# Optimization experiments

Hardware: AMD Instinct MI355X
Metric: run time of the kernel (lower is better)

## Reference

```python
import jax, jax.numpy as jnp
import numpy as np

N_X = 20000      # bessel x-grid
N_ELL = 48       # sparse tabulated multipoles
N_K = 1024       # k quadrature points
N_TAU = 600      # conformal-time samples
K_PIVOT = 0.05


def fast_interp(x, xmin, xmax, ytab):
    """Uniform-grid linear interpolation (tools.fast_interp). ytab: [Nx]."""
    n = ytab.shape[0]
    pos = jnp.clip((x - xmin) / (xmax - xmin) * (n - 1), 0.0, n - 1.0)
    i0 = jnp.clip(jnp.floor(pos).astype(jnp.int32), 0, n - 2)
    w = pos - i0
    return ytab[i0] * (1.0 - w) + ytab[i0 + 1] * w


def setup_inputs() -> dict:
    key = jax.random.key(0)
    ks = jax.random.split(key, 8)
    k = jnp.logspace(-4.0, 0.0, N_K, dtype=jnp.float32)           # Mpc^-1
    tau = jnp.linspace(50.0, 14000.0, N_TAU, dtype=jnp.float32)    # Mpc
    tau0 = jnp.asarray(14100.0, dtype=jnp.float32)
    bessel_x_tab = jnp.linspace(0.0, 15000.0, N_X, dtype=jnp.float32)
    mk = lambda kk, sh, s: (s * jax.random.normal(kk, sh, dtype=jnp.float32))
    return {
        "k": k,
        "tau": tau,
        "tau0": tau0,
        "S0": mk(ks[0], (N_K, N_TAU), 1e-2),
        "S1": mk(ks[1], (N_K, N_TAU), 1e-2),
        "S2": mk(ks[2], (N_K, N_TAU), 1e-2),
        "SE": mk(ks[3], (N_K, N_TAU), 1e-2),
        "bessel_x_tab": bessel_x_tab,
        "phi0_tab": mk(ks[4], (N_X, N_ELL), 1e-1),
        "phi1_tab": mk(ks[5], (N_X, N_ELL), 1e-1),
        "phi2_tab": mk(ks[6], (N_X, N_ELL), 1e-1),
        "eps_tab": mk(ks[7], (N_X, N_ELL), 1e-1),
        "A_s": jnp.asarray(2.1e-9, dtype=jnp.float32),
        "n_s": jnp.asarray(0.965, dtype=jnp.float32),
    }


def reference(k, tau, tau0, S0, S1, S2, SE, bessel_x_tab,
              phi0_tab, phi1_tab, phi2_tab, eps_tab, A_s, n_s):
    xmin = bessel_x_tab[0]
    xmax = bessel_x_tab[-1]
    # radial argument x = k * (tau0 - tau): [K, T]
    x = k[:, None] * (tau0 - tau)[None, :]

    def one_ell(p0, p1, p2, pe):
        # lookup phi0/phi1/phi2/epsilon at every (k, tau), fuse with sources
        srcT = (S0 * fast_interp(x, xmin, xmax, p0)
                + S1 * fast_interp(x, xmin, xmax, p1)
                + S2 * fast_interp(x, xmin, xmax, p2))
        Tl = jnp.trapezoid(srcT, tau, axis=-1)                       # [K]
        El = jnp.trapezoid(SE * fast_interp(x, xmin, xmax, pe), tau, axis=-1)
        return Tl, El

    # vmap over the tabulated-ell axis (columns of the Bessel tables)
    Tl, El = jax.vmap(one_ell, in_axes=(1, 1, 1, 1))(
        phi0_tab, phi1_tab, phi2_tab, eps_tab)                       # [L, K]

    # primordial curvature spectrum P_R(k) = A_s (k/k_p)^(n_s-1) * 2 pi^2 / k^3
    P_R = A_s * (k / K_PIVOT) ** (n_s - 1.0) * (2.0 * jnp.pi ** 2 / k ** 3)
    w = k * k * P_R                                                   # [K]
    c = 2.0 / jnp.pi
    ClTT = c * jnp.trapezoid(w * Tl * Tl, k, axis=-1)                 # [L]
    ClEE = c * jnp.trapezoid(w * El * El, k, axis=-1)
    ClTE = c * jnp.trapezoid(w * Tl * El, k, axis=-1)
    return jnp.stack([ClTT, ClEE, ClTE], axis=0)                      # [3, L]
```

## Files before the change

### kernel.cpp

```cpp
#include <hip/hip_runtime.h>
#include <math.h>

#define N_X   20000
#define N_ELL 48
#define N_K   1024
#define N_TAU 600
#define SPLIT 4
#define CHUNK (N_TAU / SPLIT)

__device__ __forceinline__ unsigned int pack_half2(float lo, float hi) {
    _Float16 l = (_Float16)lo, h = (_Float16)hi;
    unsigned short lu = __builtin_bit_cast(unsigned short, l);
    unsigned short hu = __builtin_bit_cast(unsigned short, h);
    return (unsigned int)lu | ((unsigned int)hu << 16);
}
__device__ __forceinline__ float fdot2(unsigned int a, unsigned int b, float c) {
    float d;
    asm("v_dot2_f32_f16 %0, %1, %2, %3" : "=v"(d) : "v"(a), "v"(b), "v"(c));
    return d;
}

__global__ __launch_bounds__(256) void repack_kernel(
    const float* __restrict__ p0, const float* __restrict__ p1,
    const float* __restrict__ p2, const float* __restrict__ pe,
    uint4* __restrict__ P)
{
    const int total = N_X * N_ELL;
    for (int idx = blockIdx.x * blockDim.x + threadIdx.x; idx < total;
         idx += gridDim.x * blockDim.x) {
        int x = idx / N_ELL;
        int e = idx - x * N_ELL;
        int xn = (x < N_X - 1) ? x + 1 : x;
        int a = x * N_ELL + e, b = xn * N_ELL + e;
        uint4 v;
        v.x = pack_half2(p0[a], p0[b]);
        v.y = pack_half2(p1[a], p1[b]);
        v.z = pack_half2(p2[a], p2[b]);
        v.w = pack_half2(pe[a], pe[b]);
        P[idx] = v;
    }
}

__global__ __launch_bounds__(256) void tl_el_packed(
    const float* __restrict__ k, const float* __restrict__ tau,
    const float* __restrict__ tau0p,
    const float* __restrict__ S0, const float* __restrict__ S1,
    const float* __restrict__ S2, const float* __restrict__ SE,
    const float* __restrict__ bx, const uint4* __restrict__ P,
    float* __restrict__ Tlp, float* __restrict__ Elp)
{
    const int bid  = blockIdx.x;
    const int part = bid & (SPLIT - 1);
    const int kidx = (N_K - 1) - (bid >> 2);
    const int t0   = part * CHUNK;
    const int tid  = threadIdx.x;
    const int wave = tid >> 6;
    const int lane = tid & 63;
    const int ell  = (lane < N_ELL) ? lane : (N_ELL - 1);

    __shared__ unsigned int off_s[CHUNK];
    __shared__ uint4        W2_s[CHUNK];
    __shared__ float        redT[4][N_ELL];
    __shared__ float        redE[4][N_ELL];

    const float kk    = k[kidx];
    const float tau0  = tau0p[0];
    const float xmin  = bx[0];
    const float xmax  = bx[N_X - 1];
    const float scale = (float)(N_X - 1) / (xmax - xmin);

    if (tid < CHUNK) {
        int t = t0 + tid;
        float tt = tau[t];
        float tp = (t > 0)         ? tau[t - 1] : tt;
        float tn = (t < N_TAU - 1) ? tau[t + 1] : tt;
        float wt = 0.5f * (tn - tp);
        float x   = kk * (tau0 - tt);
        float pos = (x - xmin) * scale;
        pos = fminf(fmaxf(pos, 0.0f), (float)(N_X - 1));
        int i0 = (int)pos;
        if (i0 > N_X - 2) i0 = N_X - 2;
        float w  = pos - (float)i0;
        float om = 1.0f - w;
        size_t sb = (size_t)kidx * N_TAU + t;
        float s0 = wt * S0[sb], s1 = wt * S1[sb];
        float s2 = wt * S2[sb], se = wt * SE[sb];
        uint4 w2;
        w2.x = pack_half2(s0 * om, s0 * w);
        w2.y = pack_half2(s1 * om, s1 * w);
        w2.z = pack_half2(s2 * om, s2 * w);
        w2.w = pack_half2(se * om, se * w);
        W2_s[tid]  = w2;
        off_s[tid] = (unsigned int)i0 * (N_ELL * 16u);
    }
    __syncthreads();

    const char* Pb = (const char*)P;
    const unsigned int elloff = (unsigned int)ell * 16u;
    float aT0 = 0.0f, aT1 = 0.0f, aT2 = 0.0f, aE = 0.0f;

    #pragma unroll 4
    for (int i = wave; i < CHUNK; i += 4) {
        unsigned int voff = off_s[i] + elloff;
        uint4 pr = *(const uint4*)(Pb + voff);
        uint4 w2 = W2_s[i];
        aT0 = fdot2(pr.x, w2.x, aT0);
        aT1 = fdot2(pr.y, w2.y, aT1);
        aT2 = fdot2(pr.z, w2.z, aT2);
        aE  = fdot2(pr.w, w2.w, aE);
    }
    float accT = (aT0 + aT1) + aT2;

    if (lane < N_ELL) { redT[wave][lane] = accT; redE[wave][lane] = aE; }
    __syncthreads();
    if (tid < N_ELL) {
        float sT = (redT[0][tid] + redT[1][tid]) + (redT[2][tid] + redT[3][tid]);
        float sE = (redE[0][tid] + redE[1][tid]) + (redE[2][tid] + redE[3][tid]);
        Tlp[((size_t)part * N_ELL + tid) * N_K + kidx] = sT;
        Elp[((size_t)part * N_ELL + tid) * N_K + kidx] = sE;
    }
}

__global__ __launch_bounds__(256) void tl_el_kernel(
    const float* __restrict__ k, const float* __restrict__ tau,
    const float* __restrict__ tau0p,
    const float* __restrict__ S0, const float* __restrict__ S1,
    const float* __restrict__ S2, const float* __restrict__ SE,
    const float* __restrict__ bx,
    const float* __restrict__ p0, const float* __restrict__ p1,
    const float* __restrict__ p2, const float* __restrict__ pe,
    float* __restrict__ Tl, float* __restrict__ El)
{
    const int kidx = blockIdx.x;
    const int tid  = threadIdx.x;
    const int wave = tid >> 6;
    const int lane = tid & 63;
    const int ell  = (lane < N_ELL) ? lane : (N_ELL - 1);

    const float kk    = k[kidx];
    const float tau0  = tau0p[0];
    const float xmin  = bx[0];
    const float xmax  = bx[N_X - 1];
    const float scale = (float)(N_X - 1) / (xmax - xmin);

    const float* Srow0 = S0 + (size_t)kidx * N_TAU;
    const float* Srow1 = S1 + (size_t)kidx * N_TAU;
    const float* Srow2 = S2 + (size_t)kidx * N_TAU;
    const float* SrowE = SE + (size_t)kidx * N_TAU;

    float accT = 0.0f, accE = 0.0f;

    for (int t = wave; t < N_TAU; t += 4) {
        float tt    = tau[t];
        float tprev = (t > 0)         ? tau[t - 1] : tt;
        float tnext = (t < N_TAU - 1) ? tau[t + 1] : tt;
        float wt    = 0.5f * (tnext - tprev);

        float x   = kk * (tau0 - tt);
        float pos = (x - xmin) * scale;
        pos = fminf(fmaxf(pos, 0.0f), (float)(N_X - 1));
        int i0 = (int)floorf(pos);
        if (i0 > N_X - 2) i0 = N_X - 2;
        float w = pos - (float)i0;

        int base = i0 * N_ELL + ell;
        float y00 = p0[base], y01 = p0[base + N_ELL];
        float y10 = p1[base], y11 = p1[base + N_ELL];
        float y20 = p2[base], y21 = p2[base + N_ELL];
        float ye0 = pe[base], ye1 = pe[base + N_ELL];

        float a0 = fmaf(w, y01 - y00, y00);
        float a1 = fmaf(w, y11 - y10, y10);
        float a2 = fmaf(w, y21 - y20, y20);
        float ae = fmaf(w, ye1 - ye0, ye0);

        float s0 = Srow0[t], s1 = Srow1[t], s2 = Srow2[t], se = SrowE[t];

        float srcT = s0 * a0 + s1 * a1 + s2 * a2;
        accT = fmaf(wt, srcT, accT);
        accE = fmaf(wt, se * ae, accE);
    }

    __shared__ float redT[4][N_ELL];
    __shared__ float redE[4][N_ELL];
    if (lane < N_ELL) { redT[wave][lane] = accT; redE[wave][lane] = accE; }
    __syncthreads();
    if (tid < N_ELL) {
        float sT = (redT[0][tid] + redT[1][tid]) + (redT[2][tid] + redT[3][tid]);
        float sE = (redE[0][tid] + redE[1][tid]) + (redE[2][tid] + redE[3][tid]);
        Tl[tid * N_K + kidx] = sT;
        El[tid * N_K + kidx] = sE;
    }
}

__global__ __launch_bounds__(256) void cl_kernel(
    const float* __restrict__ k,
    const float* __restrict__ Asp, const float* __restrict__ nsp,
    const float* __restrict__ Tlp, const float* __restrict__ Elp,
    int nparts, float* __restrict__ out)
{
    const int ell = blockIdx.x;
    const int tid = threadIdx.x;
    const float A_s = Asp[0];
    const float n_s = nsp[0];
    const float two_pi2 = 2.0f * (float)M_PI * (float)M_PI;

    float aTT = 0.0f, aEE = 0.0f, aTE = 0.0f;
    for (int i = tid; i < N_K; i += 256) {
        float kv    = k[i];
        float kprev = (i > 0)       ? k[i - 1] : kv;
        float knext = (i < N_K - 1) ? k[i + 1] : kv;
        float dkw   = 0.5f * (knext - kprev);
        float Pw = A_s * powf(kv / 0.05f, n_s - 1.0f) * two_pi2 / kv;
        float ww = dkw * Pw;
        float tl = 0.0f, el = 0.0f;
        for (int p = 0; p < nparts; ++p) {
            tl += Tlp[((size_t)p * N_ELL + ell) * N_K + i];
            el += Elp[((size_t)p * N_ELL + ell) * N_K + i];
        }
        aTT = fmaf(ww * tl, tl, aTT);
        aEE = fmaf(ww * el, el, aEE);
        aTE = fmaf(ww * tl, el, aTE);
    }

    for (int off = 32; off > 0; off >>= 1) {
        aTT += __shfl_down(aTT, off, 64);
        aEE += __shfl_down(aEE, off, 64);
        aTE += __shfl_down(aTE, off, 64);
    }
    __shared__ float red[3][4];
    const int wave = tid >> 6, lane = tid & 63;
    if (lane == 0) { red[0][wave] = aTT; red[1][wave] = aEE; red[2][wave] = aTE; }
    __syncthreads();
    if (tid == 0) {
        const float c = 2.0f / (float)M_PI;
        out[0 * N_ELL + ell] = c * ((red[0][0] + red[0][1]) + (red[0][2] + red[0][3]));
        out[1 * N_ELL + ell] = c * ((red[1][0] + red[1][1]) + (red[1][2] + red[1][3]));
        out[2 * N_ELL + ell] = c * ((red[2][0] + red[2][1]) + (red[2][2] + red[2][3]));
    }
}

extern "C" void kernel_launch(void* const* d_in, const int* in_sizes, int n_in,
                              void* d_out, int out_size, void* d_ws, size_t ws_size,
                              hipStream_t stream) {
    const float* k    = (const float*)d_in[0];
    const float* tau  = (const float*)d_in[1];
    const float* tau0 = (const float*)d_in[2];
    const float* S0   = (const float*)d_in[3];
    const float* S1   = (const float*)d_in[4];
    const float* S2   = (const float*)d_in[5];
    const float* SE   = (const float*)d_in[6];
    const float* bx   = (const float*)d_in[7];
    const float* p0   = (const float*)d_in[8];
    const float* p1   = (const float*)d_in[9];
    const float* p2   = (const float*)d_in[10];
    const float* pe   = (const float*)d_in[11];
    const float* A_s  = (const float*)d_in[12];
    const float* n_s  = (const float*)d_in[13];
    float* out = (float*)d_out;

    const size_t P_bytes    = (size_t)N_X * N_ELL * sizeof(uint4);
    const size_t part_bytes = (size_t)SPLIT * N_ELL * N_K * sizeof(float);

    if (ws_size >= P_bytes + 2 * part_bytes) {
        uint4* P   = (uint4*)d_ws;
        float* Tlp = (float*)((char*)d_ws + P_bytes);
        float* Elp = (float*)((char*)d_ws + P_bytes + part_bytes);

        repack_kernel<<<(N_X * N_ELL + 255) / 256, 256, 0, stream>>>(p0, p1, p2, pe, P);
        tl_el_packed<<<N_K * SPLIT, 256, 0, stream>>>(k, tau, tau0, S0, S1, S2, SE, bx,
                                                      P, Tlp, Elp);
        cl_kernel<<<N_ELL, 256, 0, stream>>>(k, A_s, n_s, Tlp, Elp, SPLIT, out);
    } else {
        float* Tl = (float*)d_ws;
        float* El = Tl + (size_t)N_ELL * N_K;
        tl_el_kernel<<<N_K, 256, 0, stream>>>(k, tau, tau0, S0, S1, S2, SE, bx,
                                              p0, p1, p2, pe, Tl, El);
        cl_kernel<<<N_ELL, 256, 0, stream>>>(k, A_s, n_s, Tl, El, 1, out);
    }
}
```

Before: 135.2 us.

## Pack Bessel tables as 8-byte rows and split Cl reduction across k-chunks

The repacked table now stores the four Bessel tables interleaved per x as half precision (8 bytes) instead of duplicating the neighbour row (16 bytes), which halves the table footprint and the repack traffic. The main kernel does two 8-byte loads (row i0 and row i0+1) and uses zero-padded dot2 weights to pull out the per-table contributions. The Cl kernel is also spread over a 2D grid of ell by k-chunk and combines partial sums with atomicAdd into an output that the repack kernel zeroes. This costs an extra load instruction per tau point and more dot2 ops, and the atomic accumulation makes the summation order nondeterministic.

```diff
diff --git a/kernel.cpp b/kernel.cpp
--- a/kernel.cpp
+++ b/kernel.cpp
@@ -7,6 +7,8 @@
 #define N_TAU 600
 #define SPLIT 4
 #define CHUNK (N_TAU / SPLIT)
+#define ROWB  (N_ELL * 8)
+#define KCH   4
 
 __device__ __forceinline__ unsigned int pack_half2(float lo, float hi) {
     _Float16 l = (_Float16)lo, h = (_Float16)hi;
@@ -20,23 +22,18 @@
     return d;
 }
 
-__global__ __launch_bounds__(256) void repack_kernel(
+__global__ __launch_bounds__(256) void repack_kernel2(
     const float* __restrict__ p0, const float* __restrict__ p1,
     const float* __restrict__ p2, const float* __restrict__ pe,
-    uint4* __restrict__ P)
-{
+    uint2* __restrict__ P, float* __restrict__ out)
+{
+    if (blockIdx.x == 0 && threadIdx.x < 3 * N_ELL) out[threadIdx.x] = 0.0f;
     const int total = N_X * N_ELL;
     for (int idx = blockIdx.x * blockDim.x + threadIdx.x; idx < total;
          idx += gridDim.x * blockDim.x) {
-        int x = idx / N_ELL;
-        int e = idx - x * N_ELL;
-        int xn = (x < N_X - 1) ? x + 1 : x;
-        int a = x * N_ELL + e, b = xn * N_ELL + e;
-        uint4 v;
-        v.x = pack_half2(p0[a], p0[b]);
-        v.y = pack_half2(p1[a], p1[b]);
-        v.z = pack_half2(p2[a], p2[b]);
-        v.w = pack_half2(pe[a], pe[b]);
+        uint2 v;
+        v.x = pack_half2(p0[idx], p1[idx]);
+        v.y = pack_half2(p2[idx], pe[idx]);
         P[idx] = v;
     }
 }
@@ -46,7 +43,7 @@
     const float* __restrict__ tau0p,
     const float* __restrict__ S0, const float* __restrict__ S1,
     const float* __restrict__ S2, const float* __restrict__ SE,
-    const float* __restrict__ bx, const uint4* __restrict__ P,
+    const float* __restrict__ bx, const uint2* __restrict__ P,
     float* __restrict__ Tlp, float* __restrict__ Elp)
 {
     const int bid  = blockIdx.x;
@@ -59,7 +56,8 @@
     const int ell  = (lane < N_ELL) ? lane : (N_ELL - 1);
 
     __shared__ unsigned int off_s[CHUNK];
-    __shared__ uint4        W2_s[CHUNK];
+    __shared__ uint4        WT_s[CHUNK];
+    __shared__ uint2        WE_s[CHUNK];
     __shared__ float        redT[4][N_ELL];
     __shared__ float        redE[4][N_ELL];
 
@@ -80,38 +78,48 @@
         pos = fminf(fmaxf(pos, 0.0f), (float)(N_X - 1));
         int i0 = (int)pos;
         if (i0 > N_X - 2) i0 = N_X - 2;
-        float w  = pos - (float)i0;
-        float om = 1.0f - w;
+        float w   = pos - (float)i0;
+        float clo = wt * (1.0f - w);
+        float chi = wt * w;
         size_t sb = (size_t)kidx * N_TAU + t;
-        float s0 = wt * S0[sb], s1 = wt * S1[sb];
-        float s2 = wt * S2[sb], se = wt * SE[sb];
-        uint4 w2;
-        w2.x = pack_half2(s0 * om, s0 * w);
-        w2.y = pack_half2(s1 * om, s1 * w);
-        w2.z = pack_half2(s2 * om, s2 * w);
-        w2.w = pack_half2(se * om, se * w);
-        W2_s[tid]  = w2;
-        off_s[tid] = (unsigned int)i0 * (N_ELL * 16u);
+        float s0 = S0[sb], s1 = S1[sb], s2 = S2[sb], se = SE[sb];
+        uint4 wt4;
+        wt4.x = pack_half2(clo * s0, clo * s1);
+        wt4.y = pack_half2(chi * s0, chi * s1);
+        wt4.z = pack_half2(clo * s2, 0.0f);
+        wt4.w = pack_half2(chi * s2, 0.0f);
+        uint2 we2;
+        we2.x = pack_half2(0.0f, clo * se);
+        we2.y = pack_half2(0.0f, chi * se);
+        WT_s[tid]  = wt4;
+        WE_s[tid]  = we2;
+        off_s[tid] = (unsigned int)i0 * (unsigned int)ROWB;
     }
     __syncthreads();
 
     const char* Pb = (const char*)P;
-    const unsigned int elloff = (unsigned int)ell * 16u;
-    float aT0 = 0.0f, aT1 = 0.0f, aT2 = 0.0f, aE = 0.0f;
+    const unsigned int elloff = (unsigned int)ell * 8u;
+    float aT0 = 0.0f, aT1 = 0.0f, aT2 = 0.0f, aT3 = 0.0f;
+    float aE0 = 0.0f, aE1 = 0.0f;
 
     #pragma unroll 4
     for (int i = wave; i < CHUNK; i += 4) {
         unsigned int voff = off_s[i] + elloff;
-        uint4 pr = *(const uint4*)(Pb + voff);
-        uint4 w2 = W2_s[i];
-        aT0 = fdot2(pr.x, w2.x, aT0);
-        aT1 = fdot2(pr.y, w2.y, aT1);
-        aT2 = fdot2(pr.z, w2.z, aT2);
-        aE  = fdot2(pr.w, w2.w, aE);
-    }
-    float accT = (aT0 + aT1) + aT2;
-
-    if (lane < N_ELL) { redT[wave][lane] = accT; redE[wave][lane] = aE; }
+        uint2 lo = *(const uint2*)(Pb + voff);
+        uint2 hi = *(const uint2*)(Pb + voff + ROWB);
+        uint4 wt4 = WT_s[i];
+        uint2 we2 = WE_s[i];
+        aT0 = fdot2(lo.x, wt4.x, aT0);
+        aT1 = fdot2(hi.x, wt4.y, aT1);
+        aT2 = fdot2(lo.y, wt4.z, aT2);
+        aT3 = fdot2(hi.y, wt4.w, aT3);
+        aE0 = fdot2(lo.y, we2.x, aE0);
+        aE1 = fdot2(hi.y, we2.y, aE1);
+    }
+    float accT = (aT0 + aT1) + (aT2 + aT3);
+    float accE = aE0 + aE1;
+
+    if (lane < N_ELL) { redT[wave][lane] = accT; redE[wave][lane] = accE; }
     __syncthreads();
     if (tid < N_ELL) {
         float sT = (redT[0][tid] + redT[1][tid]) + (redT[2][tid] + redT[3][tid]);
@@ -193,35 +201,35 @@
     }
 }
 
-__global__ __launch_bounds__(256) void cl_kernel(
+__global__ __launch_bounds__(256) void cl_kernel2(
     const float* __restrict__ k,
     const float* __restrict__ Asp, const float* __restrict__ nsp,
     const float* __restrict__ Tlp, const float* __restrict__ Elp,
     int nparts, float* __restrict__ out)
 {
-    const int ell = blockIdx.x;
-    const int tid = threadIdx.x;
+    const int ell   = blockIdx.x;
+    const int chunk = blockIdx.y;
+    const int tid   = threadIdx.x;
+    const int i     = chunk * 256 + tid;
     const float A_s = Asp[0];
     const float n_s = nsp[0];
     const float two_pi2 = 2.0f * (float)M_PI * (float)M_PI;
 
-    float aTT = 0.0f, aEE = 0.0f, aTE = 0.0f;
-    for (int i = tid; i < N_K; i += 256) {
-        float kv    = k[i];
-        float kprev = (i > 0)       ? k[i - 1] : kv;
-        float knext = (i < N_K - 1) ? k[i + 1] : kv;
-        float dkw   = 0.5f * (knext - kprev);
-        float Pw = A_s * powf(kv / 0.05f, n_s - 1.0f) * two_pi2 / kv;
-        float ww = dkw * Pw;
-        float tl = 0.0f, el = 0.0f;
-        for (int p = 0; p < nparts; ++p) {
-            tl += Tlp[((size_t)p * N_ELL + ell) * N_K + i];
-            el += Elp[((size_t)p * N_ELL + ell) * N_K + i];
-        }
-        aTT = fmaf(ww * tl, tl, aTT);
-        aEE = fmaf(ww * el, el, aEE);
-        aTE = fmaf(ww * tl, el, aTE);
-    }
+    float kv    = k[i];
+    float kprev = (i > 0)       ? k[i - 1] : kv;
+    float knext = (i < N_K - 1) ? k[i + 1] : kv;
+    float dkw   = 0.5f * (knext - kprev);
+    float Pw    = A_s * powf(kv / 0.05f, n_s - 1.0f) * two_pi2 / kv;
+    float ww    = dkw * Pw;
+
+    float tl = 0.0f, el = 0.0f;
+    for (int p = 0; p < nparts; ++p) {
+        tl += Tlp[((size_t)p * N_ELL + ell) * N_K + i];
+        el += Elp[((size_t)p * N_ELL + ell) * N_K + i];
+    }
+    float aTT = ww * tl * tl;
+    float aEE = ww * el * el;
+    float aTE = ww * tl * el;
 
     for (int off = 32; off > 0; off >>= 1) {
         aTT += __shfl_down(aTT, off, 64);
@@ -234,9 +242,12 @@
     __syncthreads();
     if (tid == 0) {
         const float c = 2.0f / (float)M_PI;
-        out[0 * N_ELL + ell] = c * ((red[0][0] + red[0][1]) + (red[0][2] + red[0][3]));
-        out[1 * N_ELL + ell] = c * ((red[1][0] + red[1][1]) + (red[1][2] + red[1][3]));
-        out[2 * N_ELL + ell] = c * ((red[2][0] + red[2][1]) + (red[2][2] + red[2][3]));
+        atomicAdd(&out[0 * N_ELL + ell],
+                  c * ((red[0][0] + red[0][1]) + (red[0][2] + red[0][3])));
+        atomicAdd(&out[1 * N_ELL + ell],
+                  c * ((red[1][0] + red[1][1]) + (red[1][2] + red[1][3])));
+        atomicAdd(&out[2 * N_ELL + ell],
+                  c * ((red[2][0] + red[2][1]) + (red[2][2] + red[2][3])));
     }
 }
 
@@ -259,23 +270,26 @@
     const float* n_s  = (const float*)d_in[13];
     float* out = (float*)d_out;
 
-    const size_t P_bytes    = (size_t)N_X * N_ELL * sizeof(uint4);
+    const size_t P_bytes    = (size_t)N_X * N_ELL * sizeof(uint2);
     const size_t part_bytes = (size_t)SPLIT * N_ELL * N_K * sizeof(float);
 
     if (ws_size >= P_bytes + 2 * part_bytes) {
-        uint4* P   = (uint4*)d_ws;
+        uint2* P   = (uint2*)d_ws;
         float* Tlp = (float*)((char*)d_ws + P_bytes);
         float* Elp = (float*)((char*)d_ws + P_bytes + part_bytes);
 
-        repack_kernel<<<(N_X * N_ELL + 255) / 256, 256, 0, stream>>>(p0, p1, p2, pe, P);
+        repack_kernel2<<<(N_X * N_ELL + 255) / 256, 256, 0, stream>>>(
+            p0, p1, p2, pe, P, out);
         tl_el_packed<<<N_K * SPLIT, 256, 0, stream>>>(k, tau, tau0, S0, S1, S2, SE, bx,
                                                       P, Tlp, Elp);
-        cl_kernel<<<N_ELL, 256, 0, stream>>>(k, A_s, n_s, Tlp, Elp, SPLIT, out);
+        cl_kernel2<<<dim3(N_ELL, KCH), 256, 0, stream>>>(k, A_s, n_s, Tlp, Elp,
+                                                         SPLIT, out);
     } else {
         float* Tl = (float*)d_ws;
         float* El = Tl + (size_t)N_ELL * N_K;
+        hipMemsetAsync(out, 0, 3 * N_ELL * sizeof(float), stream);
         tl_el_kernel<<<N_K, 256, 0, stream>>>(k, tau, tau0, S0, S1, S2, SE, bx,
                                               p0, p1, p2, pe, Tl, El);
-        cl_kernel<<<N_ELL, 256, 0, stream>>>(k, A_s, n_s, Tl, El, 1, out);
-    }
-}
+        cl_kernel2<<<dim3(N_ELL, KCH), 256, 0, stream>>>(k, A_s, n_s, Tl, El, 1, out);
+    }
+}
```

Measured after the change: 141.7 us. 1.05x slower.

## Double-buffer gather loads in tl_el and split Cl reduction across k-chunks with atomics

Applied to the files above, without the earlier changes.

The main tau loop now issues batches of eight 16-byte table gathers into two register buffers, with scheduling barriers so that loads for one batch are in flight while the previous batch is consumed. The shared arrays are padded to 160 entries with zero weights so the fixed five-batch schedule needs no bounds checks. The Cl kernel is also spread over a 2D grid of ell by k-chunk and combines its partial sums with atomicAdd into an output zeroed in the repack kernel, which raises block count for the final reduction. The cost is higher register pressure, a little wasted work on the padded entries, and a summation order that is no longer deterministic.

```diff
diff --git a/kernel.cpp b/kernel.cpp
--- a/kernel.cpp
+++ b/kernel.cpp
@@ -7,6 +7,9 @@
 #define N_TAU 600
 #define SPLIT 4
 #define CHUNK (N_TAU / SPLIT)
+#define ROWB  (N_ELL * 16)
+#define KCH   4
+#define PADN  160
 
 __device__ __forceinline__ unsigned int pack_half2(float lo, float hi) {
     _Float16 l = (_Float16)lo, h = (_Float16)hi;
@@ -23,8 +26,9 @@
 __global__ __launch_bounds__(256) void repack_kernel(
     const float* __restrict__ p0, const float* __restrict__ p1,
     const float* __restrict__ p2, const float* __restrict__ pe,
-    uint4* __restrict__ P)
+    uint4* __restrict__ P, float* __restrict__ out)
 {
+    if (blockIdx.x == 0 && threadIdx.x < 3 * N_ELL) out[threadIdx.x] = 0.0f;
     const int total = N_X * N_ELL;
     for (int idx = blockIdx.x * blockDim.x + threadIdx.x; idx < total;
          idx += gridDim.x * blockDim.x) {
@@ -58,8 +62,8 @@
     const int lane = tid & 63;
     const int ell  = (lane < N_ELL) ? lane : (N_ELL - 1);
 
-    __shared__ unsigned int off_s[CHUNK];
-    __shared__ uint4        W2_s[CHUNK];
+    __shared__ unsigned int off_s[PADN];
+    __shared__ uint4        WT_s[PADN];
     __shared__ float        redT[4][N_ELL];
     __shared__ float        redE[4][N_ELL];
 
@@ -90,8 +94,12 @@
         w2.y = pack_half2(s1 * om, s1 * w);
         w2.z = pack_half2(s2 * om, s2 * w);
         w2.w = pack_half2(se * om, se * w);
-        W2_s[tid]  = w2;
-        off_s[tid] = (unsigned int)i0 * (N_ELL * 16u);
+        WT_s[tid]  = w2;
+        off_s[tid] = (unsigned int)i0 * (unsigned int)ROWB;
+    } else if (tid < PADN) {
+        uint4 z4; z4.x = z4.y = z4.z = z4.w = 0u;
+        WT_s[tid]  = z4;
+        off_s[tid] = 0u;
     }
     __syncthreads();
 
@@ -99,16 +107,40 @@
     const unsigned int elloff = (unsigned int)ell * 16u;
     float aT0 = 0.0f, aT1 = 0.0f, aT2 = 0.0f, aE = 0.0f;
 
-    #pragma unroll 4
-    for (int i = wave; i < CHUNK; i += 4) {
-        unsigned int voff = off_s[i] + elloff;
-        uint4 pr = *(const uint4*)(Pb + voff);
-        uint4 w2 = W2_s[i];
-        aT0 = fdot2(pr.x, w2.x, aT0);
-        aT1 = fdot2(pr.y, w2.y, aT1);
-        aT2 = fdot2(pr.z, w2.z, aT2);
-        aE  = fdot2(pr.w, w2.w, aE);
-    }
+    uint4 A[8], B[8];
+
+#define ISSUE(BUF, G)                                                      \
+    _Pragma("unroll")                                                      \
+    for (int m = 0; m < 8; ++m) {                                          \
+        unsigned int voff = off_s[wave + 4 * m + 32 * (G)] + elloff;       \
+        BUF[m] = *(const uint4*)(Pb + voff);                               \
+    }
+
+#define CONSUME(BUF, G)                                                    \
+    _Pragma("unroll")                                                      \
+    for (int m = 0; m < 8; ++m) {                                          \
+        int idx = wave + 4 * m + 32 * (G);                                 \
+        uint4 w2 = WT_s[idx];                                              \
+        aT0 = fdot2(BUF[m].x, w2.x, aT0);                                  \
+        aT1 = fdot2(BUF[m].y, w2.y, aT1);                                  \
+        aT2 = fdot2(BUF[m].z, w2.z, aT2);                                  \
+        aE  = fdot2(BUF[m].w, w2.w, aE);                                   \
+    }
+
+#define SB __builtin_amdgcn_sched_barrier(0)
+
+    ISSUE(A, 0); SB;
+    ISSUE(B, 1); SB;
+    CONSUME(A, 0); ISSUE(A, 2); SB;
+    CONSUME(B, 1); ISSUE(B, 3); SB;
+    CONSUME(A, 2); ISSUE(A, 4); SB;
+    CONSUME(B, 3); SB;
+    CONSUME(A, 4);
+
+#undef ISSUE
+#undef CONSUME
+#undef SB
+
     float accT = (aT0 + aT1) + aT2;
 
     if (lane < N_ELL) { redT[wave][lane] = accT; redE[wave][lane] = aE; }
@@ -193,35 +225,35 @@
     }
 }
 
-__global__ __launch_bounds__(256) void cl_kernel(
+__global__ __launch_bounds__(256) void cl_kernel2(
     const float* __restrict__ k,
     const float* __restrict__ Asp, const float* __restrict__ nsp,
     const float* __restrict__ Tlp, const float* __restrict__ Elp,
     int nparts, float* __restrict__ out)
 {
-    const int ell = blockIdx.x;
-    const int tid = threadIdx.x;
+    const int ell   = blockIdx.x;
+    const int chunk = blockIdx.y;
+    const int tid   = threadIdx.x;
+    const int i     = chunk * 256 + tid;
     const float A_s = Asp[0];
     const float n_s = nsp[0];
     const float two_pi2 = 2.0f * (float)M_PI * (float)M_PI;
 
-    float aTT = 0.0f, aEE = 0.0f, aTE = 0.0f;
-    for (int i = tid; i < N_K; i += 256) {
-        float kv    = k[i];
-        float kprev = (i > 0)       ? k[i - 1] : kv;
-        float knext = (i < N_K - 1) ? k[i + 1] : kv;
-        float dkw   = 0.5f * (knext - kprev);
-        float Pw = A_s * powf(kv / 0.05f, n_s - 1.0f) * two_pi2 / kv;
-        float ww = dkw * Pw;
-        float tl = 0.0f, el = 0.0f;
-        for (int p = 0; p < nparts; ++p) {
-            tl += Tlp[((size_t)p * N_ELL + ell) * N_K + i];
-            el += Elp[((size_t)p * N_ELL + ell) * N_K + i];
-        }
-        aTT = fmaf(ww * tl, tl, aTT);
-        aEE = fmaf(ww * el, el, aEE);
-        aTE = fmaf(ww * tl, el, aTE);
-    }
+    float kv    = k[i];
+    float kprev = (i > 0)       ? k[i - 1] : kv;
+    float knext = (i < N_K - 1) ? k[i + 1] : kv;
+    float dkw   = 0.5f * (knext - kprev);
+    float Pw    = A_s * powf(kv / 0.05f, n_s - 1.0f) * two_pi2 / kv;
+    float ww    = dkw * Pw;
+
+    float tl = 0.0f, el = 0.0f;
+    for (int p = 0; p < nparts; ++p) {
+        tl += Tlp[((size_t)p * N_ELL + ell) * N_K + i];
+        el += Elp[((size_t)p * N_ELL + ell) * N_K + i];
+    }
+    float aTT = ww * tl * tl;
+    float aEE = ww * el * el;
+    float aTE = ww * tl * el;
 
     for (int off = 32; off > 0; off >>= 1) {
         aTT += __shfl_down(aTT, off, 64);
@@ -234,9 +266,12 @@
     __syncthreads();
     if (tid == 0) {
         const float c = 2.0f / (float)M_PI;
-        out[0 * N_ELL + ell] = c * ((red[0][0] + red[0][1]) + (red[0][2] + red[0][3]));
-        out[1 * N_ELL + ell] = c * ((red[1][0] + red[1][1]) + (red[1][2] + red[1][3]));
-        out[2 * N_ELL + ell] = c * ((red[2][0] + red[2][1]) + (red[2][2] + red[2][3]));
+        atomicAdd(&out[0 * N_ELL + ell],
+                  c * ((red[0][0] + red[0][1]) + (red[0][2] + red[0][3])));
+        atomicAdd(&out[1 * N_ELL + ell],
+                  c * ((red[1][0] + red[1][1]) + (red[1][2] + red[1][3])));
+        atomicAdd(&out[2 * N_ELL + ell],
+                  c * ((red[2][0] + red[2][1]) + (red[2][2] + red[2][3])));
     }
 }
 
@@ -267,15 +302,18 @@
         float* Tlp = (float*)((char*)d_ws + P_bytes);
         float* Elp = (float*)((char*)d_ws + P_bytes + part_bytes);
 
-        repack_kernel<<<(N_X * N_ELL + 255) / 256, 256, 0, stream>>>(p0, p1, p2, pe, P);
+        repack_kernel<<<(N_X * N_ELL + 255) / 256, 256, 0, stream>>>(
+            p0, p1, p2, pe, P, out);
         tl_el_packed<<<N_K * SPLIT, 256, 0, stream>>>(k, tau, tau0, S0, S1, S2, SE, bx,
                                                       P, Tlp, Elp);
-        cl_kernel<<<N_ELL, 256, 0, stream>>>(k, A_s, n_s, Tlp, Elp, SPLIT, out);
+        cl_kernel2<<<dim3(N_ELL, KCH), 256, 0, stream>>>(k, A_s, n_s, Tlp, Elp,
+                                                         SPLIT, out);
     } else {
         float* Tl = (float*)d_ws;
         float* El = Tl + (size_t)N_ELL * N_K;
+        hipMemsetAsync(out, 0, 3 * N_ELL * sizeof(float), stream);
         tl_el_kernel<<<N_K, 256, 0, stream>>>(k, tau, tau0, S0, S1, S2, SE, bx,
                                               p0, p1, p2, pe, Tl, El);
-        cl_kernel<<<N_ELL, 256, 0, stream>>>(k, A_s, n_s, Tl, El, 1, out);
-    }
-}
+        cl_kernel2<<<dim3(N_ELL, KCH), 256, 0, stream>>>(k, A_s, n_s, Tl, El, 1, out);
+    }
+}
```

New measurement: 129.9 us. 1.04x faster.
